# Performance work log

Hardware: AMD Instinct MI355X
Metric: run time of the kernel (lower is better)

Reference implementation:

```python
import jax, jax.numpy as jnp
import numpy as np

NEG_SLOPE = 0.01  # nn.LeakyReLU default

def _leaky(x):
    return jnp.where(x >= 0, x, NEG_SLOPE * x)

def setup_inputs() -> dict:
    key = jax.random.key(0)
    ks = jax.random.split(key, 8)
    in_ch = 64
    B, H, W = 8, 256, 256
    x = jax.random.normal(ks[0], (B, 2 * in_ch, H, W), dtype=jnp.float32)
    dims = [(64, 128), (32, 64), (16, 32), (8, 16), (4, 8), (2, 4), (1, 2)]
    inp = {"x": x}
    for i, (o, c) in enumerate(dims):
        # kaiming_normal_ fan_out, relu: std = sqrt(2 / fan_out), fan_out = o*1*1
        std = np.sqrt(2.0 / o).astype(np.float32)
        inp[f"w{i+1}"] = jax.random.normal(ks[i + 1], (o, c), dtype=jnp.float32) * std
    return inp

def reference(x, w1, w2, w3, w4, w5, w6, w7):
    # Each 1x1 conv (bias-free) is a per-pixel matmul over channels.
    h = x
    for w in (w1, w2, w3, w4, w5, w6):
        h = _leaky(jnp.einsum('bchw,oc->bohw', h, w))
    out = jnp.einsum('bchw,oc->bohw', h, w7)  # final conv, no activation
    return out
```

## Files before the change

kernel.cpp:

```cpp
#include <hip/hip_runtime.h>


#define NEG_SLOPE 0.01f
constexpr int HW = 65536;

typedef __attribute__((ext_vector_type(8))) short bf16x8;
typedef __attribute__((ext_vector_type(4))) float f32x4;
typedef __attribute__((ext_vector_type(2))) float f32x2;

__device__ __forceinline__ float leaky(float v) { return v >= 0.f ? v : NEG_SLOPE * v; }

__device__ __forceinline__ short f2b(float f) {
    unsigned u = __float_as_uint(f);
    u += 0x7fffu + ((u >> 16) & 1u);
    return (short)(u >> 16);
}
__device__ __forceinline__ unsigned pk2(float a, float b) {
    return (unsigned)(unsigned short)f2b(a) | ((unsigned)(unsigned short)f2b(b) << 16);
}

__device__ __forceinline__ bf16x8 loadA(const float* __restrict__ wsrc, int C, int m, int k) {
    f32x4 lo = *(const f32x4*)(wsrc + m * C + k);
    f32x4 hi = *(const f32x4*)(wsrc + m * C + k + 4);
    union { bf16x8 v; unsigned u[4]; } r;
    r.u[0] = pk2(lo[0], lo[1]); r.u[1] = pk2(lo[2], lo[3]);
    r.u[2] = pk2(hi[0], hi[1]); r.u[3] = pk2(hi[2], hi[3]);
    return r.v;
}

__device__ __forceinline__ void async_cp16(const float* g, float* l) {
    __builtin_amdgcn_global_load_lds((const __attribute__((address_space(1))) unsigned*)g,
                                     (__attribute__((address_space(3))) unsigned*)l,
                                     16, 0, 0);
}

__global__ __launch_bounds__(256, 2) void fused_staged_kernel(
    const float* __restrict__ x,
    const float* __restrict__ w1, const float* __restrict__ w2,
    const float* __restrict__ w3, const float* __restrict__ w4,
    const float* __restrict__ w5, const float* __restrict__ w6,
    const float* __restrict__ w7, float* __restrict__ out) {
    __shared__ float lds_x[2][32 * 128];
    __shared__ unsigned long long lds_un[4][544];
    __shared__ float lds_tw[176];

    const int tid = threadIdx.x;
    if (tid < 128)      lds_tw[tid] = w4[tid];
    else if (tid < 160) lds_tw[tid] = w5[tid - 128];
    else if (tid < 168) lds_tw[tid] = w6[tid - 160];
    else if (tid < 170) lds_tw[tid] = w7[tid - 168];

    const int w    = tid >> 6;
    const int lane = tid & 63;
    const int n    = lane & 15;
    const int q    = lane >> 4;
    const int half = lane >> 5;
    const int pl   = lane & 31;

    const int px0   = blockIdx.x * 128;
    const int batch = px0 >> 16;
    const int pin   = px0 & (HW - 1);
    const float* xg = x + (size_t)batch * 128 * HW + pin;

#pragma unroll
    for (int i = 0; i < 4; ++i) {
        int cp = w * 8 + 2 * i;
        const float* g = xg + (size_t)(cp + half) * HW + pl * 4;
        async_cp16(g, &lds_x[0][cp * 128]);
    }

    bf16x8 a1[4][4];
#pragma unroll
    for (int Mt = 0; Mt < 4; ++Mt)
#pragma unroll
        for (int kc = 0; kc < 4; ++kc)
            a1[Mt][kc] = loadA(w1, 128, Mt * 16 + n, kc * 32 + q * 8);
    bf16x8 a2[2][2];
#pragma unroll
    for (int Mt = 0; Mt < 2; ++Mt)
#pragma unroll
        for (int kc = 0; kc < 2; ++kc)
            a2[Mt][kc] = loadA(w2, 64, Mt * 16 + n, kc * 32 + q * 8);
    bf16x8 a3 = loadA(w3, 32, n, q * 8);

    __syncthreads();

    f32x4 acc1[4][2];
#pragma unroll
    for (int Mt = 0; Mt < 4; ++Mt)
#pragma unroll
        for (int Nt = 0; Nt < 2; ++Nt) acc1[Mt][Nt] = (f32x4){0.f, 0.f, 0.f, 0.f};

#pragma unroll
    for (int kc = 0; kc < 4; ++kc) {
        if (kc < 3) {
#pragma unroll
            for (int i = 0; i < 4; ++i) {
                int cp = w * 8 + 2 * i;
                const float* g = xg + (size_t)((kc + 1) * 32 + cp + half) * HW + pl * 4;
                async_cp16(g, &lds_x[(kc + 1) & 1][cp * 128]);
            }
        }
        const float* xb = &lds_x[kc & 1][0];
#pragma unroll
        for (int Nt = 0; Nt < 2; ++Nt) {
            float t[8];
#pragma unroll
            for (int j = 0; j < 8; ++j)
                t[j] = xb[(q * 8 + j) * 128 + w * 32 + Nt * 16 + n];
            union { bf16x8 v; unsigned u[4]; } b;
            b.u[0] = pk2(t[0], t[1]); b.u[1] = pk2(t[2], t[3]);
            b.u[2] = pk2(t[4], t[5]); b.u[3] = pk2(t[6], t[7]);
#pragma unroll
            for (int Mt = 0; Mt < 4; ++Mt)
                acc1[Mt][Nt] = __builtin_amdgcn_mfma_f32_16x16x32_bf16(a1[Mt][kc], b.v, acc1[Mt][Nt], 0, 0, 0);
        }
        if (kc < 3) __syncthreads();
    }

    short* h1 = (short*)&lds_un[w][0];
#pragma unroll
    for (int Mt = 0; Mt < 4; ++Mt)
#pragma unroll
        for (int Nt = 0; Nt < 2; ++Nt) {
            int px = Nt * 16 + n;
            uint2 v;
            v.x = pk2(leaky(acc1[Mt][Nt][0]), leaky(acc1[Mt][Nt][1]));
            v.y = pk2(leaky(acc1[Mt][Nt][2]), leaky(acc1[Mt][Nt][3]));
            *(uint2*)(h1 + px * 68 + Mt * 16 + q * 4) = v;
        }

    f32x4 acc2[2][2];
#pragma unroll
    for (int Mt = 0; Mt < 2; ++Mt)
#pragma unroll
        for (int Nt = 0; Nt < 2; ++Nt) acc2[Mt][Nt] = (f32x4){0.f, 0.f, 0.f, 0.f};
#pragma unroll
    for (int Nt = 0; Nt < 2; ++Nt)
#pragma unroll
        for (int kc = 0; kc < 2; ++kc) {
            int off = (Nt * 16 + n) * 68 + kc * 32 + q * 8;
            uint2 lo = *(const uint2*)(h1 + off);
            uint2 hi = *(const uint2*)(h1 + off + 4);
            union { bf16x8 v; unsigned u[4]; } b;
            b.u[0] = lo.x; b.u[1] = lo.y; b.u[2] = hi.x; b.u[3] = hi.y;
#pragma unroll
            for (int Mt = 0; Mt < 2; ++Mt)
                acc2[Mt][Nt] = __builtin_amdgcn_mfma_f32_16x16x32_bf16(a2[Mt][kc], b.v, acc2[Mt][Nt], 0, 0, 0);
        }

    short* h2 = (short*)&lds_un[w][0];
#pragma unroll
    for (int Mt = 0; Mt < 2; ++Mt)
#pragma unroll
        for (int Nt = 0; Nt < 2; ++Nt) {
            int px = Nt * 16 + n;
            uint2 v;
            v.x = pk2(leaky(acc2[Mt][Nt][0]), leaky(acc2[Mt][Nt][1]));
            v.y = pk2(leaky(acc2[Mt][Nt][2]), leaky(acc2[Mt][Nt][3]));
            *(uint2*)(h2 + px * 36 + Mt * 16 + q * 4) = v;
        }

    f32x4 acc3[2];
#pragma unroll
    for (int Nt = 0; Nt < 2; ++Nt) {
        int off = (Nt * 16 + n) * 36 + q * 8;
        uint2 lo = *(const uint2*)(h2 + off);
        uint2 hi = *(const uint2*)(h2 + off + 4);
        union { bf16x8 v; unsigned u[4]; } b;
        b.u[0] = lo.x; b.u[1] = lo.y; b.u[2] = hi.x; b.u[3] = hi.y;
        f32x4 zero = {0.f, 0.f, 0.f, 0.f};
        acc3[Nt] = __builtin_amdgcn_mfma_f32_16x16x32_bf16(a3, b.v, zero, 0, 0, 0);
    }

    float* h3 = (float*)&lds_un[w][0];
#pragma unroll
    for (int Nt = 0; Nt < 2; ++Nt) {
        int px = Nt * 16 + n;
        f32x2 va = {leaky(acc3[Nt][0]), leaky(acc3[Nt][1])};
        f32x2 vb = {leaky(acc3[Nt][2]), leaky(acc3[Nt][3])};
        *(f32x2*)(h3 + px * 18 + q * 4)     = va;
        *(f32x2*)(h3 + px * 18 + q * 4 + 2) = vb;
    }

    float hh[16];
#pragma unroll
    for (int c = 0; c < 16; ++c) hh[c] = h3[pl * 18 + c];

    float g4[8];
#pragma unroll
    for (int o = 0; o < 8; ++o) {
        float a = 0.f;
#pragma unroll
        for (int c = 0; c < 16; ++c) a = fmaf(lds_tw[o * 16 + c], hh[c], a);
        g4[o] = leaky(a);
    }
    float g5[4];
#pragma unroll
    for (int o = 0; o < 4; ++o) {
        float a = 0.f;
#pragma unroll
        for (int c = 0; c < 8; ++c) a = fmaf(lds_tw[128 + o * 8 + c], g4[c], a);
        g5[o] = leaky(a);
    }
    float g6[2];
#pragma unroll
    for (int o = 0; o < 2; ++o) {
        float a = 0.f;
#pragma unroll
        for (int c = 0; c < 4; ++c) a = fmaf(lds_tw[160 + o * 4 + c], g5[c], a);
        g6[o] = leaky(a);
    }
    float res = fmaf(lds_tw[168], g6[0], lds_tw[169] * g6[1]);
    if (lane < 32) out[px0 + w * 32 + pl] = res;
}

extern "C" void kernel_launch(void* const* d_in, const int* in_sizes, int n_in,
                              void* d_out, int out_size, void* d_ws, size_t ws_size,
                              hipStream_t stream) {
    const float* x  = (const float*)d_in[0];
    const float* w1 = (const float*)d_in[1];
    const float* w2 = (const float*)d_in[2];
    const float* w3 = (const float*)d_in[3];
    const float* w4 = (const float*)d_in[4];
    const float* w5 = (const float*)d_in[5];
    const float* w6 = (const float*)d_in[6];
    const float* w7 = (const float*)d_in[7];
    float* out = (float*)d_out;

    const int P = 8 * 256 * 256;
    fused_staged_kernel<<<P / 128, 256, 0, stream>>>(x, w1, w2, w3, w4, w5, w6, w7, out);
}
```

Baseline: 402.7 us.

## Switch to single-wave blocks with full x tile load and no barriers

Each block is now one 64-lane wave handling 64 pixels. It loads all 128 channels of its x tile into LDS up front with async copies, then waits with s_waitcnt, so the double-buffered loop and all __syncthreads are gone. The loop runs over four 16-pixel tiles and carries each through layers 1-3 with smaller accumulator sets. This removes barrier stalls but gives up the overlap between loading and compute inside a block, and each block uses about 32KB of LDS plus reloads all weights per 64 pixels, so weight traffic rises and occupancy may be limited.

```diff
diff --git a/kernel.cpp b/kernel.cpp
--- a/kernel.cpp
+++ b/kernel.cpp
@@ -6,7 +6,6 @@
 
 typedef __attribute__((ext_vector_type(8))) short bf16x8;
 typedef __attribute__((ext_vector_type(4))) float f32x4;
-typedef __attribute__((ext_vector_type(2))) float f32x2;
 
 __device__ __forceinline__ float leaky(float v) { return v >= 0.f ? v : NEG_SLOPE * v; }
 
@@ -34,39 +33,39 @@
                                      16, 0, 0);
 }
 
-__global__ __launch_bounds__(256, 2) void fused_staged_kernel(
+__global__ __launch_bounds__(64) void fused_wave_kernel(
     const float* __restrict__ x,
     const float* __restrict__ w1, const float* __restrict__ w2,
     const float* __restrict__ w3, const float* __restrict__ w4,
     const float* __restrict__ w5, const float* __restrict__ w6,
     const float* __restrict__ w7, float* __restrict__ out) {
-    __shared__ float lds_x[2][32 * 128];
-    __shared__ unsigned long long lds_un[4][544];
+    __shared__ float lds_x[128 * 64];
+    __shared__ alignas(16) short lds_h[16 * 68];
+    __shared__ float lds_h3[64 * 17];
     __shared__ float lds_tw[176];
 
-    const int tid = threadIdx.x;
-    if (tid < 128)      lds_tw[tid] = w4[tid];
-    else if (tid < 160) lds_tw[tid] = w5[tid - 128];
-    else if (tid < 168) lds_tw[tid] = w6[tid - 160];
-    else if (tid < 170) lds_tw[tid] = w7[tid - 168];
-
-    const int w    = tid >> 6;
-    const int lane = tid & 63;
+    const int lane = threadIdx.x;
     const int n    = lane & 15;
     const int q    = lane >> 4;
-    const int half = lane >> 5;
-    const int pl   = lane & 31;
 
-    const int px0   = blockIdx.x * 128;
+    const int px0   = blockIdx.x * 64;
     const int batch = px0 >> 16;
     const int pin   = px0 & (HW - 1);
     const float* xg = x + (size_t)batch * 128 * HW + pin;
 
 #pragma unroll
-    for (int i = 0; i < 4; ++i) {
-        int cp = w * 8 + 2 * i;
-        const float* g = xg + (size_t)(cp + half) * HW + pl * 4;
-        async_cp16(g, &lds_x[0][cp * 128]);
+    for (int i = 0; i < 32; ++i)
+        async_cp16(xg + (size_t)(i * 4 + q) * HW + n * 4, &lds_x[i * 256]);
+
+#pragma unroll
+    for (int t0 = 0; t0 < 3; ++t0) {
+        int t = t0 * 64 + lane;
+        float v = 0.f;
+        if (t < 128)      v = w4[t];
+        else if (t < 160) v = w5[t - 128];
+        else if (t < 168) v = w6[t - 160];
+        else if (t < 170) v = w7[t - 168];
+        if (t < 170) lds_tw[t] = v;
     }
 
     bf16x8 a1[4][4];
@@ -83,109 +82,77 @@
             a2[Mt][kc] = loadA(w2, 64, Mt * 16 + n, kc * 32 + q * 8);
     bf16x8 a3 = loadA(w3, 32, n, q * 8);
 
-    __syncthreads();
-
-    f32x4 acc1[4][2];
-#pragma unroll
-    for (int Mt = 0; Mt < 4; ++Mt)
-#pragma unroll
-        for (int Nt = 0; Nt < 2; ++Nt) acc1[Mt][Nt] = (f32x4){0.f, 0.f, 0.f, 0.f};
+    __builtin_amdgcn_s_waitcnt(0);
 
 #pragma unroll
-    for (int kc = 0; kc < 4; ++kc) {
-        if (kc < 3) {
+    for (int Nt = 0; Nt < 4; ++Nt) {
+        f32x4 acc1[4];
 #pragma unroll
-            for (int i = 0; i < 4; ++i) {
-                int cp = w * 8 + 2 * i;
-                const float* g = xg + (size_t)((kc + 1) * 32 + cp + half) * HW + pl * 4;
-                async_cp16(g, &lds_x[(kc + 1) & 1][cp * 128]);
-            }
-        }
-        const float* xb = &lds_x[kc & 1][0];
+        for (int Mt = 0; Mt < 4; ++Mt) acc1[Mt] = (f32x4){0.f, 0.f, 0.f, 0.f};
 #pragma unroll
-        for (int Nt = 0; Nt < 2; ++Nt) {
+        for (int kc = 0; kc < 4; ++kc) {
             float t[8];
 #pragma unroll
             for (int j = 0; j < 8; ++j)
-                t[j] = xb[(q * 8 + j) * 128 + w * 32 + Nt * 16 + n];
+                t[j] = lds_x[(kc * 32 + q * 8 + j) * 64 + Nt * 16 + n];
             union { bf16x8 v; unsigned u[4]; } b;
             b.u[0] = pk2(t[0], t[1]); b.u[1] = pk2(t[2], t[3]);
             b.u[2] = pk2(t[4], t[5]); b.u[3] = pk2(t[6], t[7]);
 #pragma unroll
             for (int Mt = 0; Mt < 4; ++Mt)
-                acc1[Mt][Nt] = __builtin_amdgcn_mfma_f32_16x16x32_bf16(a1[Mt][kc], b.v, acc1[Mt][Nt], 0, 0, 0);
-        }
-        if (kc < 3) __syncthreads();
-    }
-
-    short* h1 = (short*)&lds_un[w][0];
-#pragma unroll
-    for (int Mt = 0; Mt < 4; ++Mt)
-#pragma unroll
-        for (int Nt = 0; Nt < 2; ++Nt) {
-            int px = Nt * 16 + n;
-            uint2 v;
-            v.x = pk2(leaky(acc1[Mt][Nt][0]), leaky(acc1[Mt][Nt][1]));
-            v.y = pk2(leaky(acc1[Mt][Nt][2]), leaky(acc1[Mt][Nt][3]));
-            *(uint2*)(h1 + px * 68 + Mt * 16 + q * 4) = v;
+                acc1[Mt] = __builtin_amdgcn_mfma_f32_16x16x32_bf16(a1[Mt][kc], b.v, acc1[Mt], 0, 0, 0);
         }
 
-    f32x4 acc2[2][2];
 #pragma unroll
-    for (int Mt = 0; Mt < 2; ++Mt)
+        for (int Mt = 0; Mt < 4; ++Mt) {
+            uint2 v;
+            v.x = pk2(leaky(acc1[Mt][0]), leaky(acc1[Mt][1]));
+            v.y = pk2(leaky(acc1[Mt][2]), leaky(acc1[Mt][3]));
+            *(uint2*)(lds_h + n * 68 + Mt * 16 + q * 4) = v;
+        }
+
+        f32x4 acc2[2];
 #pragma unroll
-        for (int Nt = 0; Nt < 2; ++Nt) acc2[Mt][Nt] = (f32x4){0.f, 0.f, 0.f, 0.f};
-#pragma unroll
-    for (int Nt = 0; Nt < 2; ++Nt)
+        for (int Mt = 0; Mt < 2; ++Mt) acc2[Mt] = (f32x4){0.f, 0.f, 0.f, 0.f};
 #pragma unroll
         for (int kc = 0; kc < 2; ++kc) {
-            int off = (Nt * 16 + n) * 68 + kc * 32 + q * 8;
-            uint2 lo = *(const uint2*)(h1 + off);
-            uint2 hi = *(const uint2*)(h1 + off + 4);
+            const short* src = lds_h + n * 68 + kc * 32 + q * 8;
+            uint2 lo = *(const uint2*)src;
+            uint2 hi = *(const uint2*)(src + 4);
             union { bf16x8 v; unsigned u[4]; } b;
             b.u[0] = lo.x; b.u[1] = lo.y; b.u[2] = hi.x; b.u[3] = hi.y;
 #pragma unroll
             for (int Mt = 0; Mt < 2; ++Mt)
-                acc2[Mt][Nt] = __builtin_amdgcn_mfma_f32_16x16x32_bf16(a2[Mt][kc], b.v, acc2[Mt][Nt], 0, 0, 0);
+                acc2[Mt] = __builtin_amdgcn_mfma_f32_16x16x32_bf16(a2[Mt][kc], b.v, acc2[Mt], 0, 0, 0);
         }
 
-    short* h2 = (short*)&lds_un[w][0];
 #pragma unroll
-    for (int Mt = 0; Mt < 2; ++Mt)
-#pragma unroll
-        for (int Nt = 0; Nt < 2; ++Nt) {
-            int px = Nt * 16 + n;
+        for (int Mt = 0; Mt < 2; ++Mt) {
             uint2 v;
-            v.x = pk2(leaky(acc2[Mt][Nt][0]), leaky(acc2[Mt][Nt][1]));
-            v.y = pk2(leaky(acc2[Mt][Nt][2]), leaky(acc2[Mt][Nt][3]));
-            *(uint2*)(h2 + px * 36 + Mt * 16 + q * 4) = v;
+            v.x = pk2(leaky(acc2[Mt][0]), leaky(acc2[Mt][1]));
+            v.y = pk2(leaky(acc2[Mt][2]), leaky(acc2[Mt][3]));
+            *(uint2*)(lds_h + n * 36 + Mt * 16 + q * 4) = v;
         }
 
-    f32x4 acc3[2];
-#pragma unroll
-    for (int Nt = 0; Nt < 2; ++Nt) {
-        int off = (Nt * 16 + n) * 36 + q * 8;
-        uint2 lo = *(const uint2*)(h2 + off);
-        uint2 hi = *(const uint2*)(h2 + off + 4);
-        union { bf16x8 v; unsigned u[4]; } b;
-        b.u[0] = lo.x; b.u[1] = lo.y; b.u[2] = hi.x; b.u[3] = hi.y;
-        f32x4 zero = {0.f, 0.f, 0.f, 0.f};
-        acc3[Nt] = __builtin_amdgcn_mfma_f32_16x16x32_bf16(a3, b.v, zero, 0, 0, 0);
-    }
-
-    float* h3 = (float*)&lds_un[w][0];
-#pragma unroll
-    for (int Nt = 0; Nt < 2; ++Nt) {
-        int px = Nt * 16 + n;
-        f32x2 va = {leaky(acc3[Nt][0]), leaky(acc3[Nt][1])};
-        f32x2 vb = {leaky(acc3[Nt][2]), leaky(acc3[Nt][3])};
-        *(f32x2*)(h3 + px * 18 + q * 4)     = va;
-        *(f32x2*)(h3 + px * 18 + q * 4 + 2) = vb;
+        {
+            const short* src = lds_h + n * 36 + q * 8;
+            uint2 lo = *(const uint2*)src;
+            uint2 hi = *(const uint2*)(src + 4);
+            union { bf16x8 v; unsigned u[4]; } b;
+            b.u[0] = lo.x; b.u[1] = lo.y; b.u[2] = hi.x; b.u[3] = hi.y;
+            f32x4 zero = {0.f, 0.f, 0.f, 0.f};
+            f32x4 d3 = __builtin_amdgcn_mfma_f32_16x16x32_bf16(a3, b.v, zero, 0, 0, 0);
+            float* h3w = lds_h3 + (Nt * 16 + n) * 17 + q * 4;
+            h3w[0] = leaky(d3[0]);
+            h3w[1] = leaky(d3[1]);
+            h3w[2] = leaky(d3[2]);
+            h3w[3] = leaky(d3[3]);
+        }
     }
 
     float hh[16];
 #pragma unroll
-    for (int c = 0; c < 16; ++c) hh[c] = h3[pl * 18 + c];
+    for (int c = 0; c < 16; ++c) hh[c] = lds_h3[lane * 17 + c];
 
     float g4[8];
 #pragma unroll
@@ -211,8 +178,7 @@
         for (int c = 0; c < 4; ++c) a = fmaf(lds_tw[160 + o * 4 + c], g5[c], a);
         g6[o] = leaky(a);
     }
-    float res = fmaf(lds_tw[168], g6[0], lds_tw[169] * g6[1]);
-    if (lane < 32) out[px0 + w * 32 + pl] = res;
+    out[px0 + lane] = fmaf(lds_tw[168], g6[0], lds_tw[169] * g6[1]);
 }
 
 extern "C" void kernel_launch(void* const* d_in, const int* in_sizes, int n_in,
@@ -229,5 +195,5 @@
     float* out = (float*)d_out;
 
     const int P = 8 * 256 * 256;
-    fused_staged_kernel<<<P / 128, 256, 0, stream>>>(x, w1, w2, w3, w4, w5, w6, w7, out);
+    fused_wave_kernel<<<P / 64, 64, 0, stream>>>(x, w1, w2, w3, w4, w5, w6, w7, out);
 }
```

New measurement: 416.7 us. 3.5% more time.
